# Kernel optimization log

Measured on AMD Instinct MI355X. Metric: run time of the kernel, lower is better.

## Reference

```python
import jax, jax.numpy as jnp
import numpy as np

N0, N1, N2 = 20000, 15000, 15000
N = N0 + N1 + N2            # total nodes
E = 800000                  # edges (avg degree 16)
H, C = 128, 64


def setup_inputs() -> dict:
    key = jax.random.key(0)
    ks = jax.random.split(key, 16)
    s = 0.05  # weight scale
    return {
        "feat0": jax.random.normal(ks[0], (N0, 512), jnp.float32),
        "feat1": jax.random.normal(ks[1], (N1, 256), jnp.float32),
        "feat2": jax.random.normal(ks[2], (N2, 128), jnp.float32),
        "W0": jax.random.normal(ks[3], (512, H), jnp.float32) * s,
        "b0": jnp.zeros((H,), jnp.float32),
        "W1": jax.random.normal(ks[4], (256, H), jnp.float32) * s,
        "b1": jnp.zeros((H,), jnp.float32),
        "W2": jax.random.normal(ks[5], (128, H), jnp.float32) * s,
        "b2": jnp.zeros((H,), jnp.float32),
        "bias_l0": jnp.zeros((H,), jnp.float32),
        "W_l1": jax.random.normal(ks[6], (H, H), jnp.float32) * s,
        "b_l1": jnp.zeros((H,), jnp.float32),
        "W_l2": jax.random.normal(ks[7], (H, C), jnp.float32) * s,
        "b_l2": jnp.zeros((C,), jnp.float32),
        "src": jax.random.randint(ks[8], (E,), 0, N, jnp.int32),
        "dst": jax.random.randint(ks[9], (E,), 0, N, jnp.int32),
    }


def _norms(src, dst):
    # DGL GraphConv norm='both': src side uses out-degree, dst side in-degree
    ones = jnp.ones((E,), jnp.float32)
    deg_out = jax.ops.segment_sum(ones, src, num_segments=N)
    deg_in = jax.ops.segment_sum(ones, dst, num_segments=N)
    return jnp.maximum(deg_out, 1.0) ** -0.5, jnp.maximum(deg_in, 1.0) ** -0.5


def _agg(h, src, dst, norm_src, norm_dst):
    # normalized sparse aggregation: D_in^{-1/2} A D_out^{-1/2} h
    m = (h * norm_src[:, None])[src]                     # [E, d] gather
    a = jax.ops.segment_sum(m, dst, num_segments=N)      # [N, d] scatter-add
    return a * norm_dst[:, None]


def reference(feat0, feat1, feat2, W0, b0, W1, b1, W2, b2,
              bias_l0, W_l1, b_l1, W_l2, b_l2, src, dst):
    # per-node-type linear projections, concatenated along node axis
    h = jnp.concatenate([feat0 @ W0 + b0,
                         feat1 @ W1 + b1,
                         feat2 @ W2 + b2], axis=0)       # [N, H]
    ns, nd = _norms(src, dst)
    # layer 0: GraphConv(weight=False) -> agg + bias + relu (dropout = eval identity)
    h = jax.nn.relu(_agg(h, src, dst, ns, nd) + bias_l0)
    # layer 1: agg + linear + relu
    h = jax.nn.relu(_agg(h, src, dst, ns, nd) @ W_l1 + b_l1)
    # layer 2: agg + linear (no activation)
    h = _agg(h, src, dst, ns, nd) @ W_l2 + b_l2          # [N, C]
    return h
```

## Files before the change

### kernel.cpp

```cpp
#include <hip/hip_runtime.h>
#include <hip/hip_fp16.h>

#define N_NODES 50000
#define N0_ 20000
#define N1_ 15000
#define N2_ 15000
#define E_EDGES 800000
#define H_ 128
#define C_ 64

#define PB0 ((N0_ + 63) / 64)
#define PB1 ((N1_ + 63) / 64)
#define PB2 ((N2_ + 63) / 64)
#define PB_TOTAL (PB0 + PB1 + PB2)
#define EB ((E_EDGES + 255) / 256)
#define SB ((N_NODES + 255) / 256)


template <int TN, bool BIAS, bool RELU, bool SCALE, typename OT>
__device__ __forceinline__ void gemm_block(
    const float* __restrict__ A, const float* __restrict__ W,
    const float* __restrict__ bias, const float* __restrict__ rowscale,
    OT* __restrict__ out, int M, int K, int m0, float* As, float* Bs) {
    constexpr int NJ = TN / 32;
    constexpr int TN4 = TN / 4;
    int tid = threadIdx.x;
    int tx = tid & 31;
    int ty = tid >> 5;

    float acc[8][NJ];
#pragma unroll
    for (int i = 0; i < 8; i++)
#pragma unroll
        for (int j = 0; j < NJ; j++) acc[i][j] = 0.f;

    for (int k0 = 0; k0 < K; k0 += 32) {
#pragma unroll
        for (int t0 = 0; t0 < 2; t0++) {
            int t = tid + t0 * 256;
            int row = t >> 3;
            int c = t & 7;
            float4 v = make_float4(0.f, 0.f, 0.f, 0.f);
            if (m0 + row < M) v = *reinterpret_cast<const float4*>(&A[(size_t)(m0 + row) * K + k0 + c * 4]);
            As[(c * 4 + 0) * 68 + row] = v.x;
            As[(c * 4 + 1) * 68 + row] = v.y;
            As[(c * 4 + 2) * 68 + row] = v.z;
            As[(c * 4 + 3) * 68 + row] = v.w;
        }
#pragma unroll
        for (int t0 = 0; t0 < 32 * TN4 / 256; t0++) {
            int t = tid + t0 * 256;
            int r = t / TN4;
            int c4 = t % TN4;
            *reinterpret_cast<float4*>(&Bs[r * TN + c4 * 4]) =
                *reinterpret_cast<const float4*>(&W[(size_t)(k0 + r) * TN + c4 * 4]);
        }
        __syncthreads();
#pragma unroll 8
        for (int k = 0; k < 32; k++) {
            float4 a0 = *reinterpret_cast<float4*>(&As[k * 68 + ty * 8]);
            float4 a1 = *reinterpret_cast<float4*>(&As[k * 68 + ty * 8 + 4]);
            float ar[8] = {a0.x, a0.y, a0.z, a0.w, a1.x, a1.y, a1.z, a1.w};
            float br[NJ];
#pragma unroll
            for (int j = 0; j < NJ; j++) br[j] = Bs[k * TN + tx + 32 * j];
#pragma unroll
            for (int i = 0; i < 8; i++)
#pragma unroll
                for (int j = 0; j < NJ; j++) acc[i][j] = fmaf(ar[i], br[j], acc[i][j]);
        }
        __syncthreads();
    }
#pragma unroll
    for (int i = 0; i < 8; i++) {
        int row = m0 + ty * 8 + i;
        if (row < M) {
            float sc = SCALE ? rowscale[row] : 1.f;
#pragma unroll
            for (int j = 0; j < NJ; j++) {
                float v = acc[i][j] + (BIAS ? bias[tx + 32 * j] : 0.f);
                if (RELU) v = fmaxf(v, 0.f);
                v *= sc;
                out[(size_t)row * TN + tx + 32 * j] = (OT)v;
            }
        }
    }
}


__global__ __launch_bounds__(256) void k1_proj_rank(
    const float* __restrict__ feat0, const float* __restrict__ feat1, const float* __restrict__ feat2,
    const float* __restrict__ W0, const float* __restrict__ b0,
    const float* __restrict__ W1, const float* __restrict__ b1,
    const float* __restrict__ W2, const float* __restrict__ b2,
    __half* __restrict__ h0h,
    const int* __restrict__ src, const int* __restrict__ dst,
    int* __restrict__ cnt, int* __restrict__ degO, int* __restrict__ rank) {
    __shared__ float As[32 * 68];
    __shared__ float Bs[32 * 128];
    int bid = blockIdx.x;
    if (bid < PB_TOTAL) {
        const float* A; const float* Wp; const float* bp; __half* op; int M, K, m0;
        if (bid < PB0) {
            A = feat0; Wp = W0; bp = b0; op = h0h; M = N0_; K = 512; m0 = bid * 64;
        } else if (bid < PB0 + PB1) {
            A = feat1; Wp = W1; bp = b1; op = h0h + (size_t)N0_ * H_; M = N1_; K = 256;
            m0 = (bid - PB0) * 64;
        } else {
            A = feat2; Wp = W2; bp = b2; op = h0h + (size_t)(N0_ + N1_) * H_; M = N2_; K = 128;
            m0 = (bid - PB0 - PB1) * 64;
        }
        gemm_block<128, true, false, false, __half>(A, Wp, bp, nullptr, op, M, K, m0, As, Bs);
    } else {
        int e = (bid - PB_TOTAL) * 256 + threadIdx.x;
        if (e < E_EDGES) {
            rank[e] = atomicAdd(&cnt[dst[e]], 1);
            atomicAdd(&degO[src[e]], 1);
        }
    }
}


__global__ __launch_bounds__(256) void scan1_kernel(
    const int* __restrict__ cnt, int* __restrict__ pre, int* __restrict__ blocksum) {
    __shared__ int buf[256];
    int t = threadIdx.x;
    int i = blockIdx.x * 256 + t;
    int tot = (i < N_NODES) ? cnt[i] : 0;
    buf[t] = tot;
    __syncthreads();
#pragma unroll
    for (int off = 1; off < 256; off <<= 1) {
        int v = (t >= off) ? buf[t - off] : 0;
        __syncthreads();
        buf[t] += v;
        __syncthreads();
    }
    if (i < N_NODES) pre[i] = buf[t] - tot;
    if (t == 255) blocksum[blockIdx.x] = buf[255];
}

__global__ __launch_bounds__(256) void scan2_kernel(
    const int* __restrict__ blocksum, int* __restrict__ blockoff, int* __restrict__ rowptr) {
    __shared__ int buf[256];
    int t = threadIdx.x;
    int v = (t < SB) ? blocksum[t] : 0;
    buf[t] = v;
    __syncthreads();
#pragma unroll
    for (int off = 1; off < 256; off <<= 1) {
        int u = (t >= off) ? buf[t - off] : 0;
        __syncthreads();
        buf[t] += u;
        __syncthreads();
    }
    if (t < SB) blockoff[t] = buf[t] - v;
    if (t == 255) rowptr[N_NODES] = buf[255];
}

__global__ __launch_bounds__(256) void scan3_kernel(
    const int* __restrict__ cnt, const int* __restrict__ degO, const int* __restrict__ pre,
    const int* __restrict__ blockoff, int* __restrict__ rowptr,
    float* __restrict__ ns, float* __restrict__ nd) {
    int i = blockIdx.x * 256 + threadIdx.x;
    if (i < N_NODES) {
        rowptr[i] = blockoff[blockIdx.x] + pre[i];
        ns[i] = rsqrtf(fmaxf((float)degO[i], 1.0f));
        nd[i] = rsqrtf(fmaxf((float)cnt[i], 1.0f));
    }
}


__global__ __launch_bounds__(256) void k2_fill(
    const int* __restrict__ src, const int* __restrict__ dst,
    const int* __restrict__ rowptr, const int* __restrict__ rank,
    int* __restrict__ col) {
    int e = blockIdx.x * 256 + threadIdx.x;
    if (e < E_EDGES) col[rowptr[dst[e]] + rank[e]] = src[e];
}


template <int CH, int NSLOAD, int EPI, int OUTH>
__global__ __launch_bounds__(256) void agg_h_kernel(
    const __half* __restrict__ h, const int* __restrict__ rowptr,
    const int* __restrict__ col, const float* __restrict__ ns,
    const float* __restrict__ nd, const float* __restrict__ bias,
    void* __restrict__ out) {
    constexpr int L = CH / 8;
    constexpr int EPW = 64 / L;
    int node = blockIdx.x * 4 + (threadIdx.x >> 6);
    if (node >= N_NODES) return;
    int lane = threadIdx.x & 63;
    int li = lane & (L - 1);
    int g = lane / L;
    const uint4* __restrict__ h8 = (const uint4*)h;
    int beg = rowptr[node], end = rowptr[node + 1];
    float a0[8] = {0.f, 0.f, 0.f, 0.f, 0.f, 0.f, 0.f, 0.f};
    float a1[8] = {0.f, 0.f, 0.f, 0.f, 0.f, 0.f, 0.f, 0.f};
    union U8 { uint4 u; __half2 h2[4]; };
    int e = beg + g;
    for (; e + EPW < end; e += 2 * EPW) {
        int s0 = col[e], s1 = col[e + EPW];
        U8 u0, u1;
        u0.u = h8[(size_t)s0 * L + li];
        u1.u = h8[(size_t)s1 * L + li];
        float w0 = NSLOAD ? ns[s0] : 1.f;
        float w1 = NSLOAD ? ns[s1] : 1.f;
#pragma unroll
        for (int p = 0; p < 4; p++) {
            float2 f0 = __half22float2(u0.h2[p]);
            float2 f1 = __half22float2(u1.h2[p]);
            if (NSLOAD) {
                a0[2 * p] = fmaf(w0, f0.x, a0[2 * p]);
                a0[2 * p + 1] = fmaf(w0, f0.y, a0[2 * p + 1]);
                a1[2 * p] = fmaf(w1, f1.x, a1[2 * p]);
                a1[2 * p + 1] = fmaf(w1, f1.y, a1[2 * p + 1]);
            } else {
                a0[2 * p] += f0.x;
                a0[2 * p + 1] += f0.y;
                a1[2 * p] += f1.x;
                a1[2 * p + 1] += f1.y;
            }
        }
    }
    if (e < end) {
        int s = col[e];
        U8 u0;
        u0.u = h8[(size_t)s * L + li];
        float w0 = NSLOAD ? ns[s] : 1.f;
#pragma unroll
        for (int p = 0; p < 4; p++) {
            float2 f0 = __half22float2(u0.h2[p]);
            if (NSLOAD) {
                a0[2 * p] = fmaf(w0, f0.x, a0[2 * p]);
                a0[2 * p + 1] = fmaf(w0, f0.y, a0[2 * p + 1]);
            } else {
                a0[2 * p] += f0.x;
                a0[2 * p + 1] += f0.y;
            }
        }
    }
#pragma unroll
    for (int j = 0; j < 8; j++) {
        float v = a0[j] + a1[j];
#pragma unroll
        for (int off = 32; off >= L; off >>= 1) v += __shfl_xor(v, off);
        a0[j] = v;
    }
    if (lane < L) {
        float w = nd[node];
#pragma unroll
        for (int j = 0; j < 8; j++) a0[j] *= w;
        if (EPI == 1) {
            float sc = ns[node];
#pragma unroll
            for (int j = 0; j < 8; j++)
                a0[j] = fmaxf(a0[j] + bias[li * 8 + j], 0.f) * sc;
        } else if (EPI == 2) {
#pragma unroll
            for (int j = 0; j < 8; j++) a0[j] += bias[li * 8 + j];
        }
        if (OUTH) {
            union { uint4 u; __half hh[8]; } cv;
#pragma unroll
            for (int j = 0; j < 8; j++) cv.hh[j] = __float2half(a0[j]);
            ((uint4*)out)[(size_t)node * L + li] = cv.u;
        } else {
            float4* o4 = (float4*)out;
            o4[(size_t)node * (CH / 4) + li * 2] = make_float4(a0[0], a0[1], a0[2], a0[3]);
            o4[(size_t)node * (CH / 4) + li * 2 + 1] = make_float4(a0[4], a0[5], a0[6], a0[7]);
        }
    }
}


template <int TN, bool BIAS, bool RELU, bool SCALE, typename OT>
__global__ __launch_bounds__(256) void gemm_kernel(
    const float* __restrict__ A, const float* __restrict__ W,
    const float* __restrict__ bias, const float* __restrict__ rowscale,
    OT* __restrict__ out, int M, int K) {
    __shared__ float As[32 * 68];
    __shared__ float Bs[32 * TN];
    gemm_block<TN, BIAS, RELU, SCALE, OT>(A, W, bias, rowscale, out, M, K, blockIdx.x * 64, As, Bs);
}


extern "C" void kernel_launch(void* const* d_in, const int* in_sizes, int n_in,
                              void* d_out, int out_size, void* d_ws, size_t ws_size,
                              hipStream_t stream) {
    const float* feat0 = (const float*)d_in[0];
    const float* feat1 = (const float*)d_in[1];
    const float* feat2 = (const float*)d_in[2];
    const float* W0 = (const float*)d_in[3];
    const float* b0 = (const float*)d_in[4];
    const float* W1 = (const float*)d_in[5];
    const float* b1 = (const float*)d_in[6];
    const float* W2 = (const float*)d_in[7];
    const float* b2 = (const float*)d_in[8];
    const float* bias_l0 = (const float*)d_in[9];
    const float* W_l1 = (const float*)d_in[10];
    const float* b_l1 = (const float*)d_in[11];
    const float* W_l2 = (const float*)d_in[12];
    const float* b_l2 = (const float*)d_in[13];
    const int* src = (const int*)d_in[14];
    const int* dst = (const int*)d_in[15];
    float* out = (float*)d_out;

    char* ws = (char*)d_ws;
    size_t off = 0;
    auto alloc = [&](size_t bytes) {
        size_t cur = off;
        off += (bytes + 255) & ~(size_t)255;
        return cur;
    };
    size_t hA_off = alloc((size_t)N_NODES * H_ * 4);
    size_t hB_off = alloc((size_t)N_NODES * H_ * 4);
    size_t h0h_off = alloc((size_t)N_NODES * H_ * 2);
    size_t h1h_off = alloc((size_t)N_NODES * H_ * 2);
    size_t h2h_off = alloc((size_t)N_NODES * C_ * 2);
    size_t cnt_off = alloc((size_t)N_NODES * 4);
    size_t degO_off = alloc((size_t)N_NODES * 4);
    size_t ns_off = alloc((size_t)N_NODES * 4);
    size_t nd_off = alloc((size_t)N_NODES * 4);
    size_t rowptr_off = alloc((size_t)(N_NODES + 1) * 4);
    size_t rank_off = alloc((size_t)E_EDGES * 4);
    size_t col_off = alloc((size_t)E_EDGES * 4);
    size_t pre_off = alloc((size_t)N_NODES * 4);
    size_t bsum_off = alloc((size_t)SB * 4);
    size_t boff_off = alloc((size_t)SB * 4);

    float* hA = (float*)(ws + hA_off);
    float* hB = (float*)(ws + hB_off);
    __half* h0h = (__half*)(ws + h0h_off);
    __half* h1h = (__half*)(ws + h1h_off);
    __half* h2h = (__half*)(ws + h2h_off);
    int* cnt = (int*)(ws + cnt_off);
    int* degO = (int*)(ws + degO_off);
    float* ns = (float*)(ws + ns_off);
    float* nd = (float*)(ws + nd_off);
    int* rowptr = (int*)(ws + rowptr_off);
    int* rank = (int*)(ws + rank_off);
    int* col = (int*)(ws + col_off);
    int* pre = (int*)(ws + pre_off);
    int* bsum = (int*)(ws + bsum_off);
    int* boff = (int*)(ws + boff_off);

    hipMemsetAsync(ws + cnt_off, 0, ns_off - cnt_off, stream);

    k1_proj_rank<<<PB_TOTAL + EB, 256, 0, stream>>>(
        feat0, feat1, feat2, W0, b0, W1, b1, W2, b2, h0h, src, dst, cnt, degO, rank);
    scan1_kernel<<<SB, 256, 0, stream>>>(cnt, pre, bsum);
    scan2_kernel<<<1, 256, 0, stream>>>(bsum, boff, rowptr);
    scan3_kernel<<<SB, 256, 0, stream>>>(cnt, degO, pre, boff, rowptr, ns, nd);
    k2_fill<<<EB, 256, 0, stream>>>(src, dst, rowptr, rank, col);

    const int AGB = (N_NODES + 3) / 4;
    agg_h_kernel<128, 1, 1, 1><<<AGB, 256, 0, stream>>>(h0h, rowptr, col, ns, nd, bias_l0, h1h);
    agg_h_kernel<128, 0, 0, 0><<<AGB, 256, 0, stream>>>(h1h, rowptr, col, ns, nd, nullptr, hA);
    gemm_kernel<128, true, true, true, float><<<(N_NODES + 63) / 64, 256, 0, stream>>>(
        hA, W_l1, b_l1, ns, hB, N_NODES, 128);
    gemm_kernel<64, false, false, false, __half><<<(N_NODES + 63) / 64, 256, 0, stream>>>(
        hB, W_l2, nullptr, nullptr, h2h, N_NODES, 128);
    agg_h_kernel<64, 0, 2, 0><<<AGB, 256, 0, stream>>>(h2h, rowptr, col, ns, nd, b_l2, out);
}
```

Before: 258.0 us.

## Fuse CSR fill into scan, deepen gather unroll, store intermediates as fp16

```diff
diff --git a/kernel.cpp b/kernel.cpp
--- a/kernel.cpp
+++ b/kernel.cpp
@@ -16,10 +16,20 @@
 #define EB ((E_EDGES + 255) / 256)
 #define SB ((N_NODES + 255) / 256)
 
-
-template <int TN, bool BIAS, bool RELU, bool SCALE, typename OT>
+__device__ __forceinline__ float4 load_a4(const float* A, size_t idx) {
+    return *reinterpret_cast<const float4*>(&A[idx]);
+}
+__device__ __forceinline__ float4 load_a4(const __half* A, size_t idx) {
+    __half2 p0 = *reinterpret_cast<const __half2*>(&A[idx]);
+    __half2 p1 = *reinterpret_cast<const __half2*>(&A[idx + 2]);
+    float2 f0 = __half22float2(p0), f1 = __half22float2(p1);
+    return make_float4(f0.x, f0.y, f1.x, f1.y);
+}
+
+
+template <int TN, bool BIAS, bool RELU, bool SCALE, typename IT, typename OT>
 __device__ __forceinline__ void gemm_block(
-    const float* __restrict__ A, const float* __restrict__ W,
+    const IT* __restrict__ A, const float* __restrict__ W,
     const float* __restrict__ bias, const float* __restrict__ rowscale,
     OT* __restrict__ out, int M, int K, int m0, float* As, float* Bs) {
     constexpr int NJ = TN / 32;
@@ -41,7 +51,7 @@
             int row = t >> 3;
             int c = t & 7;
             float4 v = make_float4(0.f, 0.f, 0.f, 0.f);
-            if (m0 + row < M) v = *reinterpret_cast<const float4*>(&A[(size_t)(m0 + row) * K + k0 + c * 4]);
+            if (m0 + row < M) v = load_a4(A, (size_t)(m0 + row) * K + k0 + c * 4);
             As[(c * 4 + 0) * 68 + row] = v.x;
             As[(c * 4 + 1) * 68 + row] = v.y;
             As[(c * 4 + 2) * 68 + row] = v.z;
@@ -110,7 +120,7 @@
             A = feat2; Wp = W2; bp = b2; op = h0h + (size_t)(N0_ + N1_) * H_; M = N2_; K = 128;
             m0 = (bid - PB0 - PB1) * 64;
         }
-        gemm_block<128, true, false, false, __half>(A, Wp, bp, nullptr, op, M, K, m0, As, Bs);
+        gemm_block<128, true, false, false, float, __half>(A, Wp, bp, nullptr, op, M, K, m0, As, Bs);
     } else {
         int e = (bid - PB_TOTAL) * 256 + threadIdx.x;
         if (e < E_EDGES) {
@@ -158,29 +168,32 @@
     if (t == 255) rowptr[N_NODES] = buf[255];
 }
 
-__global__ __launch_bounds__(256) void scan3_kernel(
+__global__ __launch_bounds__(256) void scan3_fill_kernel(
     const int* __restrict__ cnt, const int* __restrict__ degO, const int* __restrict__ pre,
     const int* __restrict__ blockoff, int* __restrict__ rowptr,
-    float* __restrict__ ns, float* __restrict__ nd) {
-    int i = blockIdx.x * 256 + threadIdx.x;
-    if (i < N_NODES) {
-        rowptr[i] = blockoff[blockIdx.x] + pre[i];
-        ns[i] = rsqrtf(fmaxf((float)degO[i], 1.0f));
-        nd[i] = rsqrtf(fmaxf((float)cnt[i], 1.0f));
-    }
-}
-
-
-__global__ __launch_bounds__(256) void k2_fill(
+    float* __restrict__ ns, float* __restrict__ nd,
     const int* __restrict__ src, const int* __restrict__ dst,
-    const int* __restrict__ rowptr, const int* __restrict__ rank,
-    int* __restrict__ col) {
-    int e = blockIdx.x * 256 + threadIdx.x;
-    if (e < E_EDGES) col[rowptr[dst[e]] + rank[e]] = src[e];
-}
-
-
-template <int CH, int NSLOAD, int EPI, int OUTH>
+    const int* __restrict__ rank, int* __restrict__ col) {
+    int bid = blockIdx.x;
+    if (bid < SB) {
+        int i = bid * 256 + threadIdx.x;
+        if (i < N_NODES) {
+            rowptr[i] = blockoff[bid] + pre[i];
+            ns[i] = rsqrtf(fmaxf((float)degO[i], 1.0f));
+            nd[i] = rsqrtf(fmaxf((float)cnt[i], 1.0f));
+        }
+    } else {
+        int e = (bid - SB) * 256 + threadIdx.x;
+        if (e < E_EDGES) {
+            int d = dst[e];
+            int rp = blockoff[d >> 8] + pre[d];
+            col[rp + rank[e]] = src[e];
+        }
+    }
+}
+
+
+template <int CH, int NSLOAD, int EPI, int OUTH, int DEPTH>
 __global__ __launch_bounds__(256) void agg_h_kernel(
     const __half* __restrict__ h, const int* __restrict__ rowptr,
     const int* __restrict__ col, const float* __restrict__ ns,
@@ -195,54 +208,61 @@
     int g = lane / L;
     const uint4* __restrict__ h8 = (const uint4*)h;
     int beg = rowptr[node], end = rowptr[node + 1];
-    float a0[8] = {0.f, 0.f, 0.f, 0.f, 0.f, 0.f, 0.f, 0.f};
-    float a1[8] = {0.f, 0.f, 0.f, 0.f, 0.f, 0.f, 0.f, 0.f};
+    float acc[DEPTH][8];
+#pragma unroll
+    for (int d = 0; d < DEPTH; d++)
+#pragma unroll
+        for (int j = 0; j < 8; j++) acc[d][j] = 0.f;
     union U8 { uint4 u; __half2 h2[4]; };
     int e = beg + g;
-    for (; e + EPW < end; e += 2 * EPW) {
-        int s0 = col[e], s1 = col[e + EPW];
-        U8 u0, u1;
-        u0.u = h8[(size_t)s0 * L + li];
-        u1.u = h8[(size_t)s1 * L + li];
-        float w0 = NSLOAD ? ns[s0] : 1.f;
-        float w1 = NSLOAD ? ns[s1] : 1.f;
-#pragma unroll
-        for (int p = 0; p < 4; p++) {
-            float2 f0 = __half22float2(u0.h2[p]);
-            float2 f1 = __half22float2(u1.h2[p]);
-            if (NSLOAD) {
-                a0[2 * p] = fmaf(w0, f0.x, a0[2 * p]);
-                a0[2 * p + 1] = fmaf(w0, f0.y, a0[2 * p + 1]);
-                a1[2 * p] = fmaf(w1, f1.x, a1[2 * p]);
-                a1[2 * p + 1] = fmaf(w1, f1.y, a1[2 * p + 1]);
-            } else {
-                a0[2 * p] += f0.x;
-                a0[2 * p + 1] += f0.y;
-                a1[2 * p] += f1.x;
-                a1[2 * p + 1] += f1.y;
+    for (; e + (DEPTH - 1) * EPW < end; e += DEPTH * EPW) {
+        int s[DEPTH];
+        U8 u[DEPTH];
+        float w[DEPTH];
+#pragma unroll
+        for (int d = 0; d < DEPTH; d++) s[d] = col[e + d * EPW];
+#pragma unroll
+        for (int d = 0; d < DEPTH; d++) {
+            u[d].u = h8[(size_t)s[d] * L + li];
+            w[d] = NSLOAD ? ns[s[d]] : 1.f;
+        }
+#pragma unroll
+        for (int d = 0; d < DEPTH; d++)
+#pragma unroll
+            for (int p = 0; p < 4; p++) {
+                float2 f = __half22float2(u[d].h2[p]);
+                if (NSLOAD) {
+                    acc[d][2 * p] = fmaf(w[d], f.x, acc[d][2 * p]);
+                    acc[d][2 * p + 1] = fmaf(w[d], f.y, acc[d][2 * p + 1]);
+                } else {
+                    acc[d][2 * p] += f.x;
+                    acc[d][2 * p + 1] += f.y;
+                }
             }
-        }
-    }
-    if (e < end) {
+    }
+    for (; e < end; e += EPW) {
         int s = col[e];
         U8 u0;
         u0.u = h8[(size_t)s * L + li];
         float w0 = NSLOAD ? ns[s] : 1.f;
 #pragma unroll
         for (int p = 0; p < 4; p++) {
-            float2 f0 = __half22float2(u0.h2[p]);
+            float2 f = __half22float2(u0.h2[p]);
             if (NSLOAD) {
-                a0[2 * p] = fmaf(w0, f0.x, a0[2 * p]);
-                a0[2 * p + 1] = fmaf(w0, f0.y, a0[2 * p + 1]);
+                acc[0][2 * p] = fmaf(w0, f.x, acc[0][2 * p]);
+                acc[0][2 * p + 1] = fmaf(w0, f.y, acc[0][2 * p + 1]);
             } else {
-                a0[2 * p] += f0.x;
-                a0[2 * p + 1] += f0.y;
+                acc[0][2 * p] += f.x;
+                acc[0][2 * p + 1] += f.y;
             }
         }
     }
+    float a0[8];
 #pragma unroll
     for (int j = 0; j < 8; j++) {
-        float v = a0[j] + a1[j];
+        float v = acc[0][j];
+#pragma unroll
+        for (int d = 1; d < DEPTH; d++) v += acc[d][j];
 #pragma unroll
         for (int off = 32; off >= L; off >>= 1) v += __shfl_xor(v, off);
         a0[j] = v;
@@ -274,14 +294,14 @@
 }
 
 
-template <int TN, bool BIAS, bool RELU, bool SCALE, typename OT>
+template <int TN, bool BIAS, bool RELU, bool SCALE, typename IT, typename OT>
 __global__ __launch_bounds__(256) void gemm_kernel(
-    const float* __restrict__ A, const float* __restrict__ W,
+    const IT* __restrict__ A, const float* __restrict__ W,
     const float* __restrict__ bias, const float* __restrict__ rowscale,
     OT* __restrict__ out, int M, int K) {
     __shared__ float As[32 * 68];
     __shared__ float Bs[32 * TN];
-    gemm_block<TN, BIAS, RELU, SCALE, OT>(A, W, bias, rowscale, out, M, K, blockIdx.x * 64, As, Bs);
+    gemm_block<TN, BIAS, RELU, SCALE, IT, OT>(A, W, bias, rowscale, out, M, K, blockIdx.x * 64, As, Bs);
 }
 
 
@@ -313,10 +333,10 @@
         off += (bytes + 255) & ~(size_t)255;
         return cur;
     };
-    size_t hA_off = alloc((size_t)N_NODES * H_ * 4);
-    size_t hB_off = alloc((size_t)N_NODES * H_ * 4);
     size_t h0h_off = alloc((size_t)N_NODES * H_ * 2);
     size_t h1h_off = alloc((size_t)N_NODES * H_ * 2);
+    size_t hAh_off = alloc((size_t)N_NODES * H_ * 2);
+    size_t hBh_off = alloc((size_t)N_NODES * H_ * 2);
     size_t h2h_off = alloc((size_t)N_NODES * C_ * 2);
     size_t cnt_off = alloc((size_t)N_NODES * 4);
     size_t degO_off = alloc((size_t)N_NODES * 4);
@@ -329,10 +349,10 @@
     size_t bsum_off = alloc((size_t)SB * 4);
     size_t boff_off = alloc((size_t)SB * 4);
 
-    float* hA = (float*)(ws + hA_off);
-    float* hB = (float*)(ws + hB_off);
     __half* h0h = (__half*)(ws + h0h_off);
     __half* h1h = (__half*)(ws + h1h_off);
+    __half* hAh = (__half*)(ws + hAh_off);
+    __half* hBh = (__half*)(ws + hBh_off);
     __half* h2h = (__half*)(ws + h2h_off);
     int* cnt = (int*)(ws + cnt_off);
     int* degO = (int*)(ws + degO_off);
@@ -351,15 +371,15 @@
         feat0, feat1, feat2, W0, b0, W1, b1, W2, b2, h0h, src, dst, cnt, degO, rank);
     scan1_kernel<<<SB, 256, 0, stream>>>(cnt, pre, bsum);
     scan2_kernel<<<1, 256, 0, stream>>>(bsum, boff, rowptr);
-    scan3_kernel<<<SB, 256, 0, stream>>>(cnt, degO, pre, boff, rowptr, ns, nd);
-    k2_fill<<<EB, 256, 0, stream>>>(src, dst, rowptr, rank, col);
+    scan3_fill_kernel<<<SB + EB, 256, 0, stream>>>(
+        cnt, degO, pre, boff, rowptr, ns, nd, src, dst, rank, col);
 
     const int AGB = (N_NODES + 3) / 4;
-    agg_h_kernel<128, 1, 1, 1><<<AGB, 256, 0, stream>>>(h0h, rowptr, col, ns, nd, bias_l0, h1h);
-    agg_h_kernel<128, 0, 0, 0><<<AGB, 256, 0, stream>>>(h1h, rowptr, col, ns, nd, nullptr, hA);
-    gemm_kernel<128, true, true, true, float><<<(N_NODES + 63) / 64, 256, 0, stream>>>(
-        hA, W_l1, b_l1, ns, hB, N_NODES, 128);
-    gemm_kernel<64, false, false, false, __half><<<(N_NODES + 63) / 64, 256, 0, stream>>>(
-        hB, W_l2, nullptr, nullptr, h2h, N_NODES, 128);
-    agg_h_kernel<64, 0, 2, 0><<<AGB, 256, 0, stream>>>(h2h, rowptr, col, ns, nd, b_l2, out);
-}
+    agg_h_kernel<128, 1, 1, 1, 4><<<AGB, 256, 0, stream>>>(h0h, rowptr, col, ns, nd, bias_l0, h1h);
+    agg_h_kernel<128, 0, 0, 1, 4><<<AGB, 256, 0, stream>>>(h1h, rowptr, col, ns, nd, nullptr, hAh);
+    gemm_kernel<128, true, true, true, __half, __half><<<(N_NODES + 63) / 64, 256, 0, stream>>>(
+        hAh, W_l1, b_l1, ns, hBh, N_NODES, 128);
+    gemm_kernel<64, false, false, false, __half, __half><<<(N_NODES + 63) / 64, 256, 0, stream>>>(
+        hBh, W_l2, nullptr, nullptr, h2h, N_NODES, 128);
+    agg_h_kernel<64, 0, 2, 0, 2><<<AGB, 256, 0, stream>>>(h2h, rowptr, col, ns, nd, b_l2, out);
+}
```

New measurement: 272.0 us. 1.05x slower.
